# Performance work log

Measured on AMD Instinct MI355X. Metric: run time of the kernel, lower is better.

Reference implementation:

```python
import jax, jax.numpy as jnp
import numpy as np

V, D, H, T, L, M = 32000, 768, 12, 2048, 4, 64
HD = D // H
EPS = 1e-5


def _layer_norm(x, scale, bias):
    mu = x.mean(-1, keepdims=True)
    var = ((x - mu) ** 2).mean(-1, keepdims=True)
    return (x - mu) * jax.lax.rsqrt(var + EPS) * scale + bias


def setup_inputs() -> dict:
    key = jax.random.key(0)
    ks = jax.random.split(key, 12)
    f32 = jnp.float32
    inp = {
        "tokens": jax.random.randint(ks[0], (1, T), 0, V, dtype=jnp.int32),
        "emb": jax.random.normal(ks[1], (V, D), f32) * 0.05,
        "pos": jax.random.normal(ks[2], (T, D), f32) * 0.05,
        "mem": jax.random.normal(ks[3], (M, D), f32) * 0.05,
        "ln1_s": jnp.ones((L, D), f32),
        "ln1_b": jnp.zeros((L, D), f32),
        "wq": jax.random.normal(ks[4], (L, D, D), f32) * (D ** -0.5),
        "wk": jax.random.normal(ks[5], (L, D, D), f32) * (D ** -0.5),
        "wv": jax.random.normal(ks[6], (L, D, D), f32) * (D ** -0.5),
        "wo": jax.random.normal(ks[7], (L, D, D), f32) * (D ** -0.5),
        "ln2_s": jnp.ones((L, D), f32),
        "ln2_b": jnp.zeros((L, D), f32),
        "w1": jax.random.normal(ks[8], (L, 4 * D, D), f32) * (D ** -0.5),
        "b1": jnp.zeros((L, 4 * D), f32),
        "w2": jax.random.normal(ks[9], (L, D, 4 * D), f32) * ((4 * D) ** -0.5),
        "b2": jnp.zeros((L, D), f32),
        "lnm_s": jnp.ones((D,), f32),
        "lnm_b": jnp.zeros((D,), f32),
    }
    return inp


def reference(tokens, emb, pos, mem, ln1_s, ln1_b, wq, wk, wv, wo,
              ln2_s, ln2_b, w1, b1, w2, b2, lnm_s, lnm_b):
    B, Tt = tokens.shape
    x = emb[tokens] + pos[:Tt][None]                       # [B,T,D]
    x = jnp.concatenate([jnp.broadcast_to(mem, (B, M, D)), x], axis=1)  # [B,S,D]
    S = M + Tt
    causal = jnp.tril(jnp.ones((S, S), bool))              # [S,S]
    neg_inf = jnp.finfo(x.dtype).min
    scale = 1.0 / np.sqrt(HD)

    def block(h, p):
        l1s, l1b, Wq, Wk, Wv, Wo, l2s, l2b, W1, B1, W2, B2 = p
        n = _layer_norm(h, l1s, l1b)
        q = (n @ Wq.T).reshape(B, S, H, HD).transpose(0, 2, 1, 3)  # bhsd
        k = (n @ Wk.T).reshape(B, S, H, HD).transpose(0, 2, 1, 3)
        v = (n @ Wv.T).reshape(B, S, H, HD).transpose(0, 2, 1, 3)
        scores = jnp.einsum('bhqd,bhkd->bhqk', q, k) * scale
        scores = jnp.where(causal[None, None], scores, neg_inf)
        attn = jax.nn.softmax(scores, axis=-1)
        o = jnp.einsum('bhqk,bhkd->bhqd', attn, v)
        o = o.transpose(0, 2, 1, 3).reshape(B, S, D) @ Wo.T
        h = h + o
        n = _layer_norm(h, l2s, l2b)
        ff = jax.nn.gelu(n @ W1.T + B1, approximate=True) @ W2.T + B2
        return h + ff, None

    x, _ = jax.lax.scan(block, x, (ln1_s, ln1_b, wq, wk, wv, wo,
                                   ln2_s, ln2_b, w1, b1, w2, b2))
    x = _layer_norm(x, lnm_s, lnm_b)
    return x[:, -M:, :]
```

## Files before the change

kernel.cpp:

```cpp
#include <hip/hip_runtime.h>
#include <math.h>

#define S_TOT 2112
#define SPAD  2176
#define DMODEL 768
#define QKVLD 2304
#define NMEM 64
#define NHEAD 12
#define HDIM 64
#define NQT 33
#define CHUNK 9
#define NZ 4

typedef unsigned short ushort_t;
typedef __attribute__((ext_vector_type(8))) short short8;
typedef __attribute__((ext_vector_type(4))) float f32x4;

__device__ __forceinline__ ushort_t f2bf(float f) {
    unsigned int u = __builtin_bit_cast(unsigned int, f);
    u = (u + 0x7FFFu + ((u >> 16) & 1u)) >> 16;
    return (ushort_t)u;
}
__device__ __forceinline__ float bf2f(ushort_t u) {
    unsigned int x = ((unsigned int)u) << 16;
    return __builtin_bit_cast(float, x);
}

#define WAIT_LGKM() __builtin_amdgcn_s_waitcnt(0xC07F)
#define BAR()       __builtin_amdgcn_s_barrier()

__global__ __launch_bounds__(256) void cvt_all_kernel(
    const float* __restrict__ wq, const float* __restrict__ wk,
    const float* __restrict__ wv, const float* __restrict__ wo,
    const float* __restrict__ w1, const float* __restrict__ w2,
    ushort_t* __restrict__ wAll)
{
    const int DD = DMODEL * DMODEL;
    const int DF = DMODEL * 4 * DMODEL;
    const int DDv = DD / 4;
    const int DFv = DF / 4;
    const int PERLv = 4 * DDv + 2 * DFv;
    int i = blockIdx.x * 256 + threadIdx.x;
    int layer = i / PERLv;
    int r = i - layer * PERLv;
    const float* src;
    if (r < 3 * DDv) {
        if (r < DDv)          src = wq + (size_t)layer * DD + (size_t)r * 4;
        else if (r < 2 * DDv) src = wk + (size_t)layer * DD + (size_t)(r - DDv) * 4;
        else                  src = wv + (size_t)layer * DD + (size_t)(r - 2 * DDv) * 4;
    } else if (r < 4 * DDv) {
        src = wo + (size_t)layer * DD + (size_t)(r - 3 * DDv) * 4;
    } else if (r < 4 * DDv + DFv) {
        src = w1 + (size_t)layer * DF + (size_t)(r - 4 * DDv) * 4;
    } else {
        src = w2 + (size_t)layer * DF + (size_t)(r - 4 * DDv - DFv) * 4;
    }
    ushort_t* dst = wAll + (size_t)layer * PERLv * 4 + (size_t)r * 4;
    float4 v = *(const float4*)src;
    ushort4 o;
    o.x = f2bf(v.x); o.y = f2bf(v.y); o.z = f2bf(v.z); o.w = f2bf(v.w);
    *(ushort4*)dst = o;
}

__global__ __launch_bounds__(256) void embed_kernel(
    const int* __restrict__ tokens, const float* __restrict__ emb,
    const float* __restrict__ pos, const float* __restrict__ mem,
    float* __restrict__ x)
{
    int s = blockIdx.x;
    int tid = threadIdx.x;
    float* xr = x + (size_t)s * DMODEL;
    if (s >= S_TOT) {
        for (int d = tid; d < DMODEL; d += 256) xr[d] = 0.0f;
    } else if (s < NMEM) {
        const float* mr = mem + (size_t)s * DMODEL;
        for (int d = tid; d < DMODEL; d += 256) xr[d] = mr[d];
    } else {
        int t = s - NMEM;
        int tok = tokens[t];
        const float* er = emb + (size_t)tok * DMODEL;
        const float* pr = pos + (size_t)t * DMODEL;
        for (int d = tid; d < DMODEL; d += 256) xr[d] = er[d] + pr[d];
    }
}

template <typename OUT>
__global__ __launch_bounds__(256) void ln_kernel(
    const float* __restrict__ X, const float* __restrict__ g,
    const float* __restrict__ b, OUT* __restrict__ Y)
{
    __shared__ float red[8];
    int row = blockIdx.x, tid = threadIdx.x;
    int wv = tid >> 6, ln = tid & 63;
    const float* xr = X + (size_t)row * DMODEL;
    float v0 = xr[tid], v1 = xr[tid + 256], v2 = xr[tid + 512];

    float s = v0 + v1 + v2;
#pragma unroll
    for (int off = 1; off < 64; off <<= 1) s += __shfl_xor(s, off);
    if (ln == 0) red[wv] = s;
    __syncthreads();
    float mu = (red[0] + red[1] + red[2] + red[3]) * (1.0f / 768.0f);

    float d0 = v0 - mu, d1 = v1 - mu, d2 = v2 - mu;
    float q = d0 * d0 + d1 * d1 + d2 * d2;
#pragma unroll
    for (int off = 1; off < 64; off <<= 1) q += __shfl_xor(q, off);
    if (ln == 0) red[4 + wv] = q;
    __syncthreads();
    float var = (red[4] + red[5] + red[6] + red[7]) * (1.0f / 768.0f);
    float inv = rsqrtf(var + 1e-5f);

    OUT* yr = Y + (size_t)row * DMODEL;
    float o0 = d0 * inv * g[tid]       + b[tid];
    float o1 = d1 * inv * g[tid + 256] + b[tid + 256];
    float o2 = d2 * inv * g[tid + 512] + b[tid + 512];
    if constexpr (sizeof(OUT) == 2) {
        yr[tid] = f2bf(o0); yr[tid + 256] = f2bf(o1); yr[tid + 512] = f2bf(o2);
    } else {
        yr[tid] = o0; yr[tid + 256] = o1; yr[tid + 512] = o2;
    }
}

__global__ __launch_bounds__(512, 4) void gemm_mfma(
    const ushort_t* __restrict__ A, const ushort_t* __restrict__ B,
    const float* __restrict__ bias, const float* __restrict__ resid,
    void* __restrict__ Cp, int K, int ldc, int ncol0, int act, int c_bf16)
{
    __shared__ ushort_t As[2][8192];
    __shared__ ushort_t Bs[2][8192];
    int tid = threadIdx.x;
    int l = tid & 63, w = tid >> 6;
    int wr = w >> 1, wc = w & 1;

    int gx = gridDim.x;
    int nwg = gx * gridDim.y;
    int orig = blockIdx.x + gx * blockIdx.y;
    int q = nwg >> 3, r = nwg & 7;
    int xcd = orig & 7, loc = orig >> 3;
    int swz = (xcd < r ? xcd * (q + 1) : r * (q + 1) + (xcd - r) * q) + loc;
    int m0 = (swz / gx) * 128, n0 = (swz % gx) * 128;

    int kz = blockIdx.z;
    int nsplit = gridDim.z;
    int Kc = K / nsplit;
    bool split = (nsplit > 1);

    int row = tid >> 2, g = tid & 3;
    int sw0 = row * 128 + (((g)     ^ (row & 7)) << 4);
    int sw1 = row * 128 + (((g + 4) ^ (row & 7)) << 4);
    const ushort_t* Ap = A + (size_t)(m0 + row) * K + kz * Kc;
    const ushort_t* Bp = B + (size_t)(n0 + row) * K + kz * Kc;
    int go0 = g * 8, go1 = (g + 4) * 8;

    int kc = l >> 4, mr = l & 15;
    int aoff[2][2], boff[4][2];
#pragma unroll
    for (int i = 0; i < 2; ++i) {
        int rr = wr * 32 + i * 16 + mr;
#pragma unroll
        for (int kh = 0; kh < 2; ++kh)
            aoff[i][kh] = rr * 128 + (((kc + 4 * kh) ^ (rr & 7)) << 4);
    }
#pragma unroll
    for (int j = 0; j < 4; ++j) {
        int rr = wc * 64 + j * 16 + mr;
#pragma unroll
        for (int kh = 0; kh < 2; ++kh)
            boff[j][kh] = rr * 128 + (((kc + 4 * kh) ^ (rr & 7)) << 4);
    }

    f32x4 acc[2][4];
#pragma unroll
    for (int i = 0; i < 2; ++i)
#pragma unroll
        for (int j = 0; j < 4; ++j)
            acc[i][j] = (f32x4){0.f, 0.f, 0.f, 0.f};

    int nk = Kc >> 6;

    auto kstep = [&](int bi) {
        const char* bA = (const char*)As[bi];
        const char* bB = (const char*)Bs[bi];
        short8 af[2][2], bfr[4][2];
#pragma unroll
        for (int i = 0; i < 2; ++i)
#pragma unroll
            for (int kh = 0; kh < 2; ++kh)
                af[i][kh] = *(const short8*)(bA + aoff[i][kh]);
#pragma unroll
        for (int j = 0; j < 4; ++j)
#pragma unroll
            for (int kh = 0; kh < 2; ++kh)
                bfr[j][kh] = *(const short8*)(bB + boff[j][kh]);
#pragma unroll
        for (int kh = 0; kh < 2; ++kh)
#pragma unroll
            for (int i = 0; i < 2; ++i)
#pragma unroll
                for (int j = 0; j < 4; ++j)
                    acc[i][j] = __builtin_amdgcn_mfma_f32_16x16x32_bf16(af[i][kh], bfr[j][kh], acc[i][j], 0, 0, 0);
    };
    auto commit = [&](short8& a0, short8& a1, short8& b0, short8& b1, int bi, int t) {
        *(short8*)((char*)As[bi] + sw0) = a0;
        *(short8*)((char*)As[bi] + sw1) = a1;
        *(short8*)((char*)Bs[bi] + sw0) = b0;
        *(short8*)((char*)Bs[bi] + sw1) = b1;
        int ko = (t < nk ? t : nk - 1) << 6;
        a0 = *(const short8*)(Ap + ko + go0);
        a1 = *(const short8*)(Ap + ko + go1);
        b0 = *(const short8*)(Bp + ko + go0);
        b1 = *(const short8*)(Bp + ko + go1);
    };

    {
        short8 a0 = *(const short8*)(Ap + go0);
        short8 a1 = *(const short8*)(Ap + go1);
        short8 b0 = *(const short8*)(Bp + go0);
        short8 b1 = *(const short8*)(Bp + go1);
        *(short8*)((char*)As[0] + sw0) = a0;
        *(short8*)((char*)As[0] + sw1) = a1;
        *(short8*)((char*)Bs[0] + sw0) = b0;
        *(short8*)((char*)Bs[0] + sw1) = b1;
    }
    short8 oa0 = *(const short8*)(Ap + 64 + go0), oa1 = *(const short8*)(Ap + 64 + go1);
    short8 ob0 = *(const short8*)(Bp + 64 + go0), ob1 = *(const short8*)(Bp + 64 + go1);
    short8 ea0 = *(const short8*)(Ap + 128 + go0), ea1 = *(const short8*)(Ap + 128 + go1);
    short8 eb0 = *(const short8*)(Bp + 128 + go0), eb1 = *(const short8*)(Bp + 128 + go1);
    WAIT_LGKM(); BAR();

    for (int k = 0; k < nk; k += 2) {
        kstep(0);
        if (k + 1 < nk) commit(oa0, oa1, ob0, ob1, 1, k + 3);
        WAIT_LGKM(); BAR();
        if (k + 1 < nk) {
            kstep(1);
            if (k + 2 < nk) commit(ea0, ea1, eb0, eb1, 0, k + 4);
            WAIT_LGKM(); BAR();
        }
    }

    int lq = l >> 4;
#pragma unroll
    for (int i = 0; i < 2; ++i) {
#pragma unroll
        for (int rr = 0; rr < 4; ++rr) {
            int m = m0 + wr * 32 + i * 16 + lq * 4 + rr;
#pragma unroll
            for (int j = 0; j < 4; ++j) {
                int n = n0 + wc * 64 + j * 16 + mr;
                float v = acc[i][j][rr];
                if (bias && (!split || kz == 0)) v += bias[n];
                if (act) {
                    float u = v;
                    float t = 0.7978845608028654f * (u + 0.044715f * u * u * u);
                    v = u / (1.0f + __expf(-2.0f * t));
                }
                size_t idx = (size_t)m * ldc + ncol0 + n;
                if (split) {
                    atomicAdd((float*)Cp + idx, v);
                } else {
                    if (resid) v += resid[idx];
                    if (c_bf16) ((ushort_t*)Cp)[idx] = f2bf(v);
                    else        ((float*)Cp)[idx] = v;
                }
            }
        }
    }
}

__global__ __launch_bounds__(256) void attn_mfma(
    const ushort_t* __restrict__ qkv, ushort_t* __restrict__ Opart,
    float* __restrict__ ml)
{
    __shared__ ushort_t Qs[64][72];
    __shared__ ushort_t Ks[2][64][72];
    __shared__ ushort_t Vt[2][64][72];
    __shared__ ushort_t Ps[64][72];

    int qt = blockIdx.x;
    int h  = blockIdx.y;
    int z  = blockIdx.z;
    int kt0 = z * CHUNK;
    if (kt0 > qt) return;
    int kt1 = min(kt0 + CHUNK, qt + 1);

    int tid = threadIdx.x;
    int w = tid >> 6, lane = tid & 63;
    int quad = lane >> 4, l16 = lane & 15;
    int sr = lane;
    int dg = w;

    const size_t TSTRIDE = (size_t)64 * QKVLD;

    {
        const ushort_t* qp = qkv + (size_t)(qt * 64 + sr) * QKVLD + h * HDIM + dg * 16;
        *(short8*)&Qs[sr][dg * 16]     = *(const short8*)qp;
        *(short8*)&Qs[sr][dg * 16 + 8] = *(const short8*)(qp + 8);
    }

    const ushort_t* kp = qkv + (size_t)(kt0 * 64 + sr) * QKVLD + DMODEL + h * HDIM + dg * 16;
    const ushort_t* vp = kp + DMODEL;
    short8 pk0 = *(const short8*)kp, pk1 = *(const short8*)(kp + 8);
    short8 pv0 = *(const short8*)vp, pv1 = *(const short8*)(vp + 8);
    kp += TSTRIDE; vp += TSTRIDE;

    *(short8*)&Ks[0][sr][dg * 16]     = pk0;
    *(short8*)&Ks[0][sr][dg * 16 + 8] = pk1;
#pragma unroll
    for (int j = 0; j < 8; ++j) Vt[0][dg * 16 + j][sr] = (ushort_t)pv0[j];
#pragma unroll
    for (int j = 0; j < 8; ++j) Vt[0][dg * 16 + 8 + j][sr] = (ushort_t)pv1[j];

    pk0 = *(const short8*)kp; pk1 = *(const short8*)(kp + 8);
    pv0 = *(const short8*)vp; pv1 = *(const short8*)(vp + 8);
    kp += TSTRIDE; vp += TSTRIDE;

    WAIT_LGKM(); BAR();

    short8 qf[2];
    qf[0] = *(const short8*)&Qs[w * 16 + l16][quad * 8];
    qf[1] = *(const short8*)&Qs[w * 16 + l16][32 + quad * 8];

    float mstate[4] = {-1e30f, -1e30f, -1e30f, -1e30f};
    float lstate[4] = {0.f, 0.f, 0.f, 0.f};
    f32x4 accO[4];
#pragma unroll
    for (int j = 0; j < 4; ++j) accO[j] = (f32x4){0.f, 0.f, 0.f, 0.f};

    for (int kt = kt0; kt < kt1; ++kt) {
        int cb = (kt - kt0) & 1;

        f32x4 sacc[4];
#pragma unroll
        for (int nt = 0; nt < 4; ++nt) {
            sacc[nt] = (f32x4){0.f, 0.f, 0.f, 0.f};
            short8 kf0 = *(const short8*)&Ks[cb][nt * 16 + l16][quad * 8];
            short8 kf1 = *(const short8*)&Ks[cb][nt * 16 + l16][32 + quad * 8];
            sacc[nt] = __builtin_amdgcn_mfma_f32_16x16x32_bf16(qf[0], kf0, sacc[nt], 0, 0, 0);
            sacc[nt] = __builtin_amdgcn_mfma_f32_16x16x32_bf16(qf[1], kf1, sacc[nt], 0, 0, 0);
        }

        if (kt + 1 < kt1) {
            int nb = cb ^ 1;
            *(short8*)&Ks[nb][sr][dg * 16]     = pk0;
            *(short8*)&Ks[nb][sr][dg * 16 + 8] = pk1;
#pragma unroll
            for (int j = 0; j < 8; ++j) Vt[nb][dg * 16 + j][sr] = (ushort_t)pv0[j];
#pragma unroll
            for (int j = 0; j < 8; ++j) Vt[nb][dg * 16 + 8 + j][sr] = (ushort_t)pv1[j];
            pk0 = *(const short8*)kp; pk1 = *(const short8*)(kp + 8);
            pv0 = *(const short8*)vp; pv1 = *(const short8*)(vp + 8);
            kp += TSTRIDE; vp += TSTRIDE;
        }

        bool diag = (kt == qt);
        float s[4][4], rmax[4];
#pragma unroll
        for (int r = 0; r < 4; ++r) rmax[r] = -1e30f;
#pragma unroll
        for (int nt = 0; nt < 4; ++nt)
#pragma unroll
            for (int r = 0; r < 4; ++r) {
                float v = sacc[nt][r] * 0.125f;
                if (diag && (nt * 16 + l16) > (w * 16 + quad * 4 + r)) v = -1e30f;
                s[nt][r] = v;
                rmax[r] = fmaxf(rmax[r], v);
            }
#pragma unroll
        for (int r = 0; r < 4; ++r) {
            rmax[r] = fmaxf(rmax[r], __shfl_xor(rmax[r], 1));
            rmax[r] = fmaxf(rmax[r], __shfl_xor(rmax[r], 2));
            rmax[r] = fmaxf(rmax[r], __shfl_xor(rmax[r], 4));
            rmax[r] = fmaxf(rmax[r], __shfl_xor(rmax[r], 8));
        }
        float alpha[4];
#pragma unroll
        for (int r = 0; r < 4; ++r) {
            float mnew = fmaxf(mstate[r], rmax[r]);
            alpha[r] = __expf(mstate[r] - mnew);
            mstate[r] = mnew;
        }
        float rsum[4] = {0.f, 0.f, 0.f, 0.f};
#pragma unroll
        for (int nt = 0; nt < 4; ++nt)
#pragma unroll
            for (int r = 0; r < 4; ++r) {
                float p = __expf(s[nt][r] - mstate[r]);
                Ps[w * 16 + quad * 4 + r][nt * 16 + l16] = f2bf(p);
                rsum[r] += p;
            }
#pragma unroll
        for (int r = 0; r < 4; ++r) {
            rsum[r] += __shfl_xor(rsum[r], 1);
            rsum[r] += __shfl_xor(rsum[r], 2);
            rsum[r] += __shfl_xor(rsum[r], 4);
            rsum[r] += __shfl_xor(rsum[r], 8);
            lstate[r] = lstate[r] * alpha[r] + rsum[r];
        }
#pragma unroll
        for (int j = 0; j < 4; ++j)
#pragma unroll
            for (int r = 0; r < 4; ++r) accO[j][r] *= alpha[r];

        short8 pf0 = *(const short8*)&Ps[w * 16 + l16][quad * 8];
        short8 pf1 = *(const short8*)&Ps[w * 16 + l16][32 + quad * 8];
#pragma unroll
        for (int j = 0; j < 4; ++j) {
            short8 vf0 = *(const short8*)&Vt[cb][j * 16 + l16][quad * 8];
            short8 vf1 = *(const short8*)&Vt[cb][j * 16 + l16][32 + quad * 8];
            accO[j] = __builtin_amdgcn_mfma_f32_16x16x32_bf16(pf0, vf0, accO[j], 0, 0, 0);
            accO[j] = __builtin_amdgcn_mfma_f32_16x16x32_bf16(pf1, vf1, accO[j], 0, 0, 0);
        }

        WAIT_LGKM(); BAR();
    }

    size_t pidx = (size_t)(h * NQT + qt) * NZ + z;
#pragma unroll
    for (int j = 0; j < 4; ++j)
#pragma unroll
        for (int r = 0; r < 4; ++r) {
            int row = w * 16 + quad * 4 + r;
            Opart[pidx * 4096 + row * 64 + j * 16 + l16] = f2bf(accO[j][r]);
        }
    if (l16 == 0) {
        float* mlr = ml + pidx * 128;
#pragma unroll
        for (int r = 0; r < 4; ++r) {
            int row = w * 16 + quad * 4 + r;
            mlr[row * 2]     = mstate[r];
            mlr[row * 2 + 1] = lstate[r];
        }
    }
}

__global__ __launch_bounds__(256) void attn_combine(
    const ushort_t* __restrict__ Opart, const float* __restrict__ ml,
    ushort_t* __restrict__ att)
{
    int qt = blockIdx.x, h = blockIdx.y;
    int nch = (qt + CHUNK) / CHUNK;
    int t = threadIdx.x;
    int row = t >> 2, c0 = (t & 3) << 4;
    size_t pb = (size_t)(h * NQT + qt) * NZ;

    float mv[NZ], lv[NZ];
    float M = -1e30f;
#pragma unroll
    for (int z = 0; z < NZ; ++z) {
        mv[z] = -1e30f; lv[z] = 0.f;
        if (z < nch) {
            const float* p = ml + (pb + z) * 128 + row * 2;
            mv[z] = p[0]; lv[z] = p[1];
            M = fmaxf(M, mv[z]);
        }
    }
    float denom = 0.f;
    float sc[NZ];
#pragma unroll
    for (int z = 0; z < NZ; ++z) {
        sc[z] = 0.f;
        if (z < nch) { sc[z] = __expf(mv[z] - M); denom += sc[z] * lv[z]; }
    }
    float inv = 1.0f / denom;

    float o[16];
#pragma unroll
    for (int i = 0; i < 16; ++i) o[i] = 0.f;
#pragma unroll
    for (int z = 0; z < NZ; ++z) {
        if (z < nch) {
            const ushort_t* op = Opart + (pb + z) * 4096 + row * 64 + c0;
            short8 a0 = *(const short8*)op;
            short8 a1 = *(const short8*)(op + 8);
#pragma unroll
            for (int i = 0; i < 8; ++i) o[i]     += sc[z] * bf2f((ushort_t)a0[i]);
#pragma unroll
            for (int i = 0; i < 8; ++i) o[i + 8] += sc[z] * bf2f((ushort_t)a1[i]);
        }
    }
    ushort_t* dst = att + (size_t)(qt * 64 + row) * DMODEL + h * HDIM + c0;
    short8 r0, r1;
#pragma unroll
    for (int i = 0; i < 8; ++i) {
        r0[i] = (short)f2bf(o[i] * inv);
        r1[i] = (short)f2bf(o[i + 8] * inv);
    }
    *(short8*)dst = r0;
    *(short8*)(dst + 8) = r1;
}

extern "C" void kernel_launch(void* const* d_in, const int* in_sizes, int n_in,
                              void* d_out, int out_size, void* d_ws, size_t ws_size,
                              hipStream_t stream) {
    const int*   tokens = (const int*)d_in[0];
    const float* emb    = (const float*)d_in[1];
    const float* pos    = (const float*)d_in[2];
    const float* mem    = (const float*)d_in[3];
    const float* ln1_s  = (const float*)d_in[4];
    const float* ln1_b  = (const float*)d_in[5];
    const float* wq     = (const float*)d_in[6];
    const float* wk     = (const float*)d_in[7];
    const float* wv     = (const float*)d_in[8];
    const float* wo     = (const float*)d_in[9];
    const float* ln2_s  = (const float*)d_in[10];
    const float* ln2_b  = (const float*)d_in[11];
    const float* w1     = (const float*)d_in[12];
    const float* b1     = (const float*)d_in[13];
    const float* w2     = (const float*)d_in[14];
    const float* b2     = (const float*)d_in[15];
    const float* lnm_s  = (const float*)d_in[16];
    const float* lnm_b  = (const float*)d_in[17];
    float* out = (float*)d_out;

    const int D = DMODEL, L = 4, FF = 4 * DMODEL, SP = SPAD;
    const int DD = D * D;
    const int DF = D * FF;
    const size_t PERL = (size_t)4 * DD + 2 * DF;

    float*    x    = (float*)d_ws;
    ushort_t* qkvb = (ushort_t*)(x + (size_t)SP * D);
    ushort_t* nbuf = qkvb + (size_t)SP * 3 * D;
    ushort_t* attb = nbuf + (size_t)SP * D;
    ushort_t* ffh  = attb + (size_t)SP * D;
    ushort_t* wAll = ffh  + (size_t)SP * FF;
    ushort_t* Opart = ffh;
    float*    mlbuf = (float*)nbuf;

    embed_kernel<<<SP, 256, 0, stream>>>(tokens, emb, pos, mem, x);
    cvt_all_kernel<<<(4 * (4 * DD + 2 * DF)) / 1024, 256, 0, stream>>>(
        wq, wk, wv, wo, w1, w2, wAll);

    dim3 gQKV(18, 17);
    dim3 gO(6, 17, 4);
    dim3 gF1(24, 17);
    dim3 gF2(6, 17, 4);
    dim3 gA(NQT, NHEAD, NZ);
    dim3 gC(NQT, NHEAD);

    for (int l = 0; l < L; ++l) {
        ushort_t* wqkv = wAll + (size_t)l * PERL;
        ushort_t* wob  = wqkv + (size_t)3 * DD;
        ushort_t* w1b  = wob  + (size_t)DD;
        ushort_t* w2b  = w1b  + (size_t)DF;

        ln_kernel<ushort_t><<<SP, 256, 0, stream>>>(x, ln1_s + l * D, ln1_b + l * D, nbuf);
        gemm_mfma<<<gQKV, 512, 0, stream>>>(nbuf, wqkv, nullptr, nullptr,
                                            qkvb, D, 3 * D, 0, 0, 1);
        attn_mfma<<<gA, 256, 0, stream>>>(qkvb, Opart, mlbuf);
        attn_combine<<<gC, 256, 0, stream>>>(Opart, mlbuf, attb);
        gemm_mfma<<<gO, 512, 0, stream>>>(attb, wob, nullptr, nullptr,
                                          x, D, D, 0, 0, 0);
        ln_kernel<ushort_t><<<SP, 256, 0, stream>>>(x, ln2_s + l * D, ln2_b + l * D, nbuf);
        gemm_mfma<<<gF1, 512, 0, stream>>>(nbuf, w1b, b1 + (size_t)l * FF, nullptr,
                                           ffh, D, FF, 0, 1, 1);
        gemm_mfma<<<gF2, 512, 0, stream>>>(ffh, w2b, b2 + (size_t)l * D, nullptr,
                                           x, FF, D, 0, 0, 0);
    }
    ln_kernel<float><<<NMEM, 256, 0, stream>>>(x + (size_t)(S_TOT - NMEM) * D,
                                               lnm_s, lnm_b, out);
}
```

Before: 878.9 us.

## Rewrite GEMM to use direct global-to-LDS loads with 256-thread blocks

Rewrites the bf16 MFMA GEMM to stage tiles with global_load_lds (direct global-to-LDS DMA) instead of loading through registers and writing to shared memory. The K-step shrinks from 64 to 32, and the swizzle is changed to match. The block goes from 512 to 256 threads, so each wave now computes a 64x64 sub-tile with a 4x4 MFMA accumulator set. This is meant to cut the register and VALU cost of staging and to raise per-wave MFMA reuse. In exchange it adds more barriers per K (one per 32-wide step) and uses more accumulator registers per thread.

After: 1.019 ms. +16.0%, slower.

```diff
diff --git a/kernel.cpp b/kernel.cpp
--- a/kernel.cpp
+++ b/kernel.cpp
@@ -24,6 +24,13 @@
 __device__ __forceinline__ float bf2f(ushort_t u) {
     unsigned int x = ((unsigned int)u) << 16;
     return __builtin_bit_cast(float, x);
+}
+
+__device__ __forceinline__ void gl_lds16(const ushort_t* g, ushort_t* s) {
+    __builtin_amdgcn_global_load_lds(
+        (const __attribute__((address_space(1))) unsigned int*)g,
+        (__attribute__((address_space(3))) unsigned int*)s,
+        16, 0, 0);
 }
 
 #define WAIT_LGKM() __builtin_amdgcn_s_waitcnt(0xC07F)
@@ -122,13 +129,13 @@
     }
 }
 
-__global__ __launch_bounds__(512, 4) void gemm_mfma(
+__global__ __launch_bounds__(256, 4) void gemm_mfma(
     const ushort_t* __restrict__ A, const ushort_t* __restrict__ B,
     const float* __restrict__ bias, const float* __restrict__ resid,
     void* __restrict__ Cp, int K, int ldc, int ncol0, int act, int c_bf16)
 {
-    __shared__ ushort_t As[2][8192];
-    __shared__ ushort_t Bs[2][8192];
+    __shared__ ushort_t As[2][4096];
+    __shared__ ushort_t Bs[2][4096];
     int tid = threadIdx.x;
     int l = tid & 63, w = tid >> 6;
     int wr = w >> 1, wc = w & 1;
@@ -146,106 +153,71 @@
     int Kc = K / nsplit;
     bool split = (nsplit > 1);
 
-    int row = tid >> 2, g = tid & 3;
-    int sw0 = row * 128 + (((g)     ^ (row & 7)) << 4);
-    int sw1 = row * 128 + (((g + 4) ^ (row & 7)) << 4);
-    const ushort_t* Ap = A + (size_t)(m0 + row) * K + kz * Kc;
-    const ushort_t* Bp = B + (size_t)(n0 + row) * K + kz * Kc;
-    int go0 = g * 8, go1 = (g + 4) * 8;
+    int lrow = l >> 2;
+    int r0 = w * 32, r1 = w * 32 + 16;
+    int grow0 = r0 + lrow, grow1 = r1 + lrow;
+    int gc0 = (l & 3) ^ ((grow0 >> 1) & 3);
+    int gc1 = (l & 3) ^ ((grow1 >> 1) & 3);
+    const ushort_t* ApS0 = A + (size_t)(m0 + grow0) * K + kz * Kc + gc0 * 8;
+    const ushort_t* ApS1 = A + (size_t)(m0 + grow1) * K + kz * Kc + gc1 * 8;
+    const ushort_t* BpS0 = B + (size_t)(n0 + grow0) * K + kz * Kc + gc0 * 8;
+    const ushort_t* BpS1 = B + (size_t)(n0 + grow1) * K + kz * Kc + gc1 * 8;
+    int lb0 = r0 * 32, lb1 = r1 * 32;
 
     int kc = l >> 4, mr = l & 15;
-    int aoff[2][2], boff[4][2];
-#pragma unroll
-    for (int i = 0; i < 2; ++i) {
-        int rr = wr * 32 + i * 16 + mr;
-#pragma unroll
-        for (int kh = 0; kh < 2; ++kh)
-            aoff[i][kh] = rr * 128 + (((kc + 4 * kh) ^ (rr & 7)) << 4);
-    }
-#pragma unroll
-    for (int j = 0; j < 4; ++j) {
-        int rr = wc * 64 + j * 16 + mr;
-#pragma unroll
-        for (int kh = 0; kh < 2; ++kh)
-            boff[j][kh] = rr * 128 + (((kc + 4 * kh) ^ (rr & 7)) << 4);
-    }
-
-    f32x4 acc[2][4];
-#pragma unroll
-    for (int i = 0; i < 2; ++i)
+    int aoff[4], boff[4];
+#pragma unroll
+    for (int i = 0; i < 4; ++i) {
+        int rr = wr * 64 + i * 16 + mr;
+        aoff[i] = rr * 64 + ((kc ^ ((rr >> 1) & 3)) << 4);
+        rr = wc * 64 + i * 16 + mr;
+        boff[i] = rr * 64 + ((kc ^ ((rr >> 1) & 3)) << 4);
+    }
+
+    f32x4 acc[4][4];
+#pragma unroll
+    for (int i = 0; i < 4; ++i)
 #pragma unroll
         for (int j = 0; j < 4; ++j)
             acc[i][j] = (f32x4){0.f, 0.f, 0.f, 0.f};
 
-    int nk = Kc >> 6;
-
-    auto kstep = [&](int bi) {
-        const char* bA = (const char*)As[bi];
-        const char* bB = (const char*)Bs[bi];
-        short8 af[2][2], bfr[4][2];
-#pragma unroll
-        for (int i = 0; i < 2; ++i)
-#pragma unroll
-            for (int kh = 0; kh < 2; ++kh)
-                af[i][kh] = *(const short8*)(bA + aoff[i][kh]);
-#pragma unroll
-        for (int j = 0; j < 4; ++j)
-#pragma unroll
-            for (int kh = 0; kh < 2; ++kh)
-                bfr[j][kh] = *(const short8*)(bB + boff[j][kh]);
-#pragma unroll
-        for (int kh = 0; kh < 2; ++kh)
-#pragma unroll
-            for (int i = 0; i < 2; ++i)
-#pragma unroll
-                for (int j = 0; j < 4; ++j)
-                    acc[i][j] = __builtin_amdgcn_mfma_f32_16x16x32_bf16(af[i][kh], bfr[j][kh], acc[i][j], 0, 0, 0);
+    int nk = Kc >> 5;
+
+    auto stage = [&](int bi, int kt) {
+        int ko = kt << 5;
+        gl_lds16(ApS0 + ko, &As[bi][lb0]);
+        gl_lds16(ApS1 + ko, &As[bi][lb1]);
+        gl_lds16(BpS0 + ko, &Bs[bi][lb0]);
+        gl_lds16(BpS1 + ko, &Bs[bi][lb1]);
     };
-    auto commit = [&](short8& a0, short8& a1, short8& b0, short8& b1, int bi, int t) {
-        *(short8*)((char*)As[bi] + sw0) = a0;
-        *(short8*)((char*)As[bi] + sw1) = a1;
-        *(short8*)((char*)Bs[bi] + sw0) = b0;
-        *(short8*)((char*)Bs[bi] + sw1) = b1;
-        int ko = (t < nk ? t : nk - 1) << 6;
-        a0 = *(const short8*)(Ap + ko + go0);
-        a1 = *(const short8*)(Ap + ko + go1);
-        b0 = *(const short8*)(Bp + ko + go0);
-        b1 = *(const short8*)(Bp + ko + go1);
-    };
-
-    {
-        short8 a0 = *(const short8*)(Ap + go0);
-        short8 a1 = *(const short8*)(Ap + go1);
-        short8 b0 = *(const short8*)(Bp + go0);
-        short8 b1 = *(const short8*)(Bp + go1);
-        *(short8*)((char*)As[0] + sw0) = a0;
-        *(short8*)((char*)As[0] + sw1) = a1;
-        *(short8*)((char*)Bs[0] + sw0) = b0;
-        *(short8*)((char*)Bs[0] + sw1) = b1;
-    }
-    short8 oa0 = *(const short8*)(Ap + 64 + go0), oa1 = *(const short8*)(Ap + 64 + go1);
-    short8 ob0 = *(const short8*)(Bp + 64 + go0), ob1 = *(const short8*)(Bp + 64 + go1);
-    short8 ea0 = *(const short8*)(Ap + 128 + go0), ea1 = *(const short8*)(Ap + 128 + go1);
-    short8 eb0 = *(const short8*)(Bp + 128 + go0), eb1 = *(const short8*)(Bp + 128 + go1);
-    WAIT_LGKM(); BAR();
-
-    for (int k = 0; k < nk; k += 2) {
-        kstep(0);
-        if (k + 1 < nk) commit(oa0, oa1, ob0, ob1, 1, k + 3);
-        WAIT_LGKM(); BAR();
-        if (k + 1 < nk) {
-            kstep(1);
-            if (k + 2 < nk) commit(ea0, ea1, eb0, eb1, 0, k + 4);
-            WAIT_LGKM(); BAR();
-        }
+
+    stage(0, 0);
+    __syncthreads();
+
+    for (int k = 0; k < nk; ++k) {
+        if (k + 1 < nk) stage((k + 1) & 1, k + 1);
+        const char* bA = (const char*)As[k & 1];
+        const char* bB = (const char*)Bs[k & 1];
+        short8 af[4], bfr[4];
+#pragma unroll
+        for (int i = 0; i < 4; ++i) {
+            af[i]  = *(const short8*)(bA + aoff[i]);
+            bfr[i] = *(const short8*)(bB + boff[i]);
+        }
+#pragma unroll
+        for (int i = 0; i < 4; ++i)
+#pragma unroll
+            for (int j = 0; j < 4; ++j)
+                acc[i][j] = __builtin_amdgcn_mfma_f32_16x16x32_bf16(af[i], bfr[j], acc[i][j], 0, 0, 0);
+        __syncthreads();
     }
 
     int lq = l >> 4;
 #pragma unroll
-    for (int i = 0; i < 2; ++i) {
+    for (int i = 0; i < 4; ++i) {
 #pragma unroll
         for (int rr = 0; rr < 4; ++rr) {
-            int m = m0 + wr * 32 + i * 16 + lq * 4 + rr;
+            int m = m0 + wr * 64 + i * 16 + lq * 4 + rr;
 #pragma unroll
             for (int j = 0; j < 4; ++j) {
                 int n = n0 + wc * 64 + j * 16 + mr;
@@ -546,16 +518,16 @@
         ushort_t* w2b  = w1b  + (size_t)DF;
 
         ln_kernel<ushort_t><<<SP, 256, 0, stream>>>(x, ln1_s + l * D, ln1_b + l * D, nbuf);
-        gemm_mfma<<<gQKV, 512, 0, stream>>>(nbuf, wqkv, nullptr, nullptr,
+        gemm_mfma<<<gQKV, 256, 0, stream>>>(nbuf, wqkv, nullptr, nullptr,
                                             qkvb, D, 3 * D, 0, 0, 1);
         attn_mfma<<<gA, 256, 0, stream>>>(qkvb, Opart, mlbuf);
         attn_combine<<<gC, 256, 0, stream>>>(Opart, mlbuf, attb);
-        gemm_mfma<<<gO, 512, 0, stream>>>(attb, wob, nullptr, nullptr,
+        gemm_mfma<<<gO, 256, 0, stream>>>(attb, wob, nullptr, nullptr,
                                           x, D, D, 0, 0, 0);
         ln_kernel<ushort_t><<<SP, 256, 0, stream>>>(x, ln2_s + l * D, ln2_b + l * D, nbuf);
-        gemm_mfma<<<gF1, 512, 0, stream>>>(nbuf, w1b, b1 + (size_t)l * FF, nullptr,
+        gemm_mfma<<<gF1, 256, 0, stream>>>(nbuf, w1b, b1 + (size_t)l * FF, nullptr,
                                            ffh, D, FF, 0, 1, 1);
-        gemm_mfma<<<gF2, 512, 0, stream>>>(ffh, w2b, b2 + (size_t)l * D, nullptr,
+        gemm_mfma<<<gF2, 256, 0, stream>>>(ffh, w2b, b2 + (size_t)l * D, nullptr,
                                            x, FF, D, 0, 0, 0);
     }
     ln_kernel<float><<<NMEM, 256, 0, stream>>>(x + (size_t)(S_TOT - NMEM) * D,
```
